# Kernel optimization log

Measured on AMD Instinct MI355X. Metric: run time of the kernel, lower is better.

## Reference

```python
import jax, jax.numpy as jnp
import numpy as np

N = 20000          # total nodes across batched graphs
E_REL = 60000      # edges per relation type (3 relation types)
N_CLASSES = 32
NUM_GRAPHS = 64
HEADS = 8
OUT_CH = 48
FUSED = 384        # 3 * 128 fused node feature dim
EPS = 1e-5         # PyG LayerNorm eps
NEG_SLOPE = 0.2    # RGATConv leaky_relu slope
NUM_ITERS = 2


def setup_inputs() -> dict:
    key = jax.random.key(0)
    ks = iter(jax.random.split(key, 48))

    def nrm(shape, scale=0.05):
        return jax.random.normal(next(ks), shape, jnp.float32) * scale

    inp = {}
    inp["x_visual"] = jax.random.normal(next(ks), (N, 1024), jnp.float32)
    inp["x_geom"] = jax.random.normal(next(ks), (N, 6), jnp.float32)
    inp["x_prior"] = jax.random.uniform(next(ks), (N, N_CLASSES + 1), jnp.float32)
    inp["edge_index_overlap"] = jax.random.randint(next(ks), (2, E_REL), 0, N)
    inp["edge_index_arch"] = jax.random.randint(next(ks), (2, E_REL), 0, N)
    inp["edge_index_spatial"] = jax.random.randint(next(ks), (2, E_REL), 0, N)
    inp["batch"] = jnp.sort(jax.random.randint(next(ks), (N,), 0, NUM_GRAPHS))
    # encoders: Linear -> ReLU -> PyG LayerNorm(graph mode, batch=None)
    inp["vis_W"] = nrm((1024, 128)); inp["vis_b"] = jnp.zeros((128,), jnp.float32)
    inp["vis_lnw"] = jnp.ones((128,), jnp.float32); inp["vis_lnb"] = jnp.zeros((128,), jnp.float32)
    inp["geo_W"] = nrm((6, 128)); inp["geo_b"] = jnp.zeros((128,), jnp.float32)
    inp["geo_lnw"] = jnp.ones((128,), jnp.float32); inp["geo_lnb"] = jnp.zeros((128,), jnp.float32)
    inp["pri_W"] = nrm((N_CLASSES + 1, 128)); inp["pri_b"] = jnp.zeros((128,), jnp.float32)
    inp["pri_lnw"] = jnp.ones((128,), jnp.float32); inp["pri_lnb"] = jnp.zeros((128,), jnp.float32)
    # RGATConv params: weight (R, in, H*O), q/k (H*O, H*dim) with dim=1, bias (H*O)
    for i in (1, 2):
        inp[f"rgat{i}_W"] = nrm((3, FUSED, HEADS * OUT_CH))
        inp[f"rgat{i}_q"] = nrm((HEADS * OUT_CH, HEADS))
        inp[f"rgat{i}_k"] = nrm((HEADS * OUT_CH, HEADS))
        inp[f"rgat{i}_bias"] = jnp.zeros((HEADS * OUT_CH,), jnp.float32)
        inp[f"n{i}_w"] = jnp.ones((FUSED,), jnp.float32)
        inp[f"n{i}_b"] = jnp.zeros((FUSED,), jnp.float32)
    inp["cls_W1"] = nrm((FUSED, 128)); inp["cls_b1"] = jnp.zeros((128,), jnp.float32)
    inp["cls_W2"] = nrm((128, N_CLASSES)); inp["cls_b2"] = jnp.zeros((N_CLASSES,), jnp.float32)
    return inp


def _encoder(x, W, b, lnw, lnb):
    # Linear -> ReLU -> PyG LayerNorm(mode='graph', batch=None): scalar mean/std
    h = jax.nn.relu(x @ W + b)
    h = h - h.mean()
    h = h / (h.std() + EPS)
    return h * lnw + lnb


def _graph_layernorm(x, batch, w, b):
    # PyG LayerNorm(mode='graph') with batch vector: normalize per graph over nodes*channels
    cnt = jax.ops.segment_sum(jnp.ones((x.shape[0],), x.dtype), batch, NUM_GRAPHS)
    norm = jnp.clip(cnt, 1.0, None) * x.shape[-1]
    mean = jax.ops.segment_sum(x, batch, NUM_GRAPHS).sum(-1) / norm
    xc = x - mean[batch][:, None]
    var = jax.ops.segment_sum(xc * xc, batch, NUM_GRAPHS).sum(-1) / norm
    out = xc / jnp.sqrt(var + EPS)[batch][:, None]
    return out * w + b


def _rgat(x, src, dst, etype, W, q, k, bias):
    # RGATConv: additive self-attention, across-relation softmax, concat heads, sum aggr
    n = x.shape[0]
    xr = jnp.einsum('nf,rfo->rno', x, W)          # per-relation node transform (R,N,H*O)
    outi = xr[etype, dst]                          # (E, H*O) transformed dst features
    outj = xr[etype, src]                          # (E, H*O) transformed src features
    alpha = jax.nn.leaky_relu(outi @ q + outj @ k, NEG_SLOPE)  # (E, H)
    amax = jax.ops.segment_max(alpha, dst, n)
    amax = jnp.where(jnp.isfinite(amax), amax, 0.0)
    ex = jnp.exp(alpha - amax[dst])
    den = jax.ops.segment_sum(ex, dst, n)
    a = ex / (den[dst] + 1e-16)                    # per-dst-node softmax over all relations
    msg = (a[:, :, None] * outj.reshape(-1, HEADS, OUT_CH)).reshape(-1, HEADS * OUT_CH)
    return jax.ops.segment_sum(msg, dst, n) + bias


def reference(x_visual, x_geom, x_prior, edge_index_overlap, edge_index_arch,
              edge_index_spatial, batch, vis_W, vis_b, vis_lnw, vis_lnb,
              geo_W, geo_b, geo_lnw, geo_lnb, pri_W, pri_b, pri_lnw, pri_lnb,
              rgat1_W, rgat1_q, rgat1_k, rgat1_bias, n1_w, n1_b,
              rgat2_W, rgat2_q, rgat2_k, rgat2_bias, n2_w, n2_b,
              cls_W1, cls_b1, cls_W2, cls_b2):
    ei = jnp.concatenate([edge_index_overlap, edge_index_arch, edge_index_spatial], axis=1)
    src, dst = ei[0], ei[1]
    etype = jnp.concatenate([jnp.full((E_REL,), r, jnp.int32) for r in range(3)])

    h_vis = _encoder(x_visual, vis_W, vis_b, vis_lnw, vis_lnb)
    h_geo = _encoder(x_geom, geo_W, geo_b, geo_lnw, geo_lnb)

    cur_prior = x_prior
    logits = None
    for t in range(NUM_ITERS):
        h_pri = _encoder(cur_prior, pri_W, pri_b, pri_lnw, pri_lnb)
        h0 = jnp.concatenate([h_vis, h_geo, h_pri], axis=-1)  # (N, 384)
        h1 = jax.nn.elu(_rgat(h0, src, dst, etype, rgat1_W, rgat1_q, rgat1_k, rgat1_bias)) + h0
        h1 = _graph_layernorm(h1, batch, n1_w, n1_b)
        h2 = jax.nn.elu(_rgat(h1, src, dst, etype, rgat2_W, rgat2_q, rgat2_k, rgat2_bias)) + h1
        h2 = _graph_layernorm(h2, batch, n2_w, n2_b)
        logits = jax.nn.relu(h2 @ cls_W1 + cls_b1) @ cls_W2 + cls_b2  # dropout off (eval)
        if t < NUM_ITERS - 1:
            probs = jax.nn.softmax(logits, axis=-1)
            cur_prior = jnp.concatenate([probs, probs.max(-1, keepdims=True)], axis=-1)
    return logits
```

## Files before the change

kernel.cpp:

```cpp
#include <hip/hip_runtime.h>
#include <hip/hip_bf16.h>

#define Nn 20000
#define EREL 60000
#define ETOT 180000
#define NG 64
#define FD 384
#define EPS 1e-5f

typedef unsigned short u16;
typedef unsigned int u32;
typedef __attribute__((ext_vector_type(8))) short s8v;
typedef __attribute__((ext_vector_type(4))) float f4v;

static inline int cdiv(int a, int b) { return (a + b - 1) / b; }

__device__ inline u16 f2b(float f) {
    __hip_bfloat16 h = __float2bfloat16(f);
    union { __hip_bfloat16 b; u16 u; } c; c.b = h; return c.u;
}
__device__ inline float b2f(u16 u) {
    union { __hip_bfloat16 b; u16 u; } c; c.u = u; return __bfloat162float(c.b);
}

template<bool WLO>
__global__ __launch_bounds__(256) void split_k(const float* __restrict__ x,
    u16* __restrict__ hi, u16* __restrict__ lo, int n4)
{
    int i = blockIdx.x * 256 + threadIdx.x;
    if (i >= n4) return;
    float4 v = ((const float4*)x)[i];
    ushort4 h;
    h.x = f2b(v.x); h.y = f2b(v.y); h.z = f2b(v.z); h.w = f2b(v.w);
    ((ushort4*)hi)[i] = h;
    if (WLO) {
        ushort4 l;
        l.x = f2b(v.x - b2f(h.x));
        l.y = f2b(v.y - b2f(h.y));
        l.z = f2b(v.z - b2f(h.z));
        l.w = f2b(v.w - b2f(h.w));
        ((ushort4*)lo)[i] = l;
    }
}

template<bool WLO>
__global__ void tsplit_k(const float* __restrict__ W, u16* __restrict__ hi,
                         u16* __restrict__ lo, int K, int N, int total)
{
    int idx = blockIdx.x * 256 + threadIdx.x;
    if (idx >= total) return;
    int kn = K * N;
    int b = idx / kn, rem = idx - b * kn;
    int k = rem / N, n = rem - k * N;
    float v = W[idx];
    u16 h = f2b(v);
    int o = b * kn + n * K + k;
    hi[o] = h;
    if (WLO) lo[o] = f2b(v - b2f(h));
}

__global__ __launch_bounds__(256) void w2_k(const float* __restrict__ W0,
    const float* __restrict__ q0, const float* __restrict__ k0,
    const float* __restrict__ W1, const float* __restrict__ q1, const float* __restrict__ k1,
    u16* __restrict__ hi, u16* __restrict__ lo)
{
    int idx = blockIdx.x * 256 + threadIdx.x;
    if (idx >= 2 * 3 * 384 * 16) return;
    int c = idx & 15;
    int rest = idx >> 4;
    int kin = rest % 384;
    int lr3 = rest / 384;
    int L = lr3 / 3, r = lr3 - L * 3;
    const float* W = (L ? W1 : W0) + ((size_t)r * 384 + kin) * 384;
    const float* qm = (c < 8) ? (L ? q1 : q0) : (L ? k1 : k0);
    int h = c & 7;
    float s = 0.f;
    for (int d = 0; d < 384; d++) s = fmaf(W[d], qm[d * 8 + h], s);
    u16 hh = f2b(s);
    size_t o = ((size_t)L * 48 + r * 16 + c) * 384 + kin;
    hi[o] = hh;
    lo[o] = f2b(s - b2f(hh));
}

#define USEI(i) ((i) < 2 || ((i) >= 4 && (i) < 6) || (TERMS >= 2 && ((i) == 2 || (i) == 3)) || (TERMS >= 3 && (i) >= 6))
template<bool BIAS, bool RELU, bool STATS, bool OB16, int TERMS, bool SWZ>
__global__ __launch_bounds__(256) void mgemm_k(
    const u16* __restrict__ Ahi, const u16* __restrict__ Alo,
    const u16* __restrict__ Bhi, const u16* __restrict__ Blo,
    const float* __restrict__ bias, void* __restrict__ Cv,
    int M, int K, int ldc, int bstride, float* __restrict__ stats)
{
    __shared__ u16 lds[4 * 128 * 32];
    __shared__ float red[256];
    const int t = threadIdx.x;
    int brow, bcol, z;
    if (SWZ) {
        int d = blockIdx.x;
        int xcd = d & 7, s = d >> 3;
        int row = xcd + 8 * (s / 9);
        int c = s % 9;
        brow = row * 128;
        if (brow >= M) return;
        bcol = (c % 3) * 128;
        z = c / 3;
    } else {
        brow = blockIdx.x * 128; bcol = blockIdx.y * 128; z = blockIdx.z;
    }
    Bhi += (size_t)z * bstride;
    Blo += (size_t)z * bstride;
    float* Cf = OB16 ? nullptr : (float*)Cv + (size_t)z * M * ldc;
    u16*   Ch = OB16 ? (u16*)Cv + (size_t)z * M * ldc : nullptr;

    const int r0 = t >> 2, sl = t & 3;
    const int rA0 = min(brow + r0, M - 1);
    const int rA1 = min(brow + r0 + 64, M - 1);
    const u16* gsrc[8];
    gsrc[0] = Ahi + (size_t)rA0 * K + sl * 8;
    gsrc[1] = Ahi + (size_t)rA1 * K + sl * 8;
    gsrc[2] = Alo + (size_t)rA0 * K + sl * 8;
    gsrc[3] = Alo + (size_t)rA1 * K + sl * 8;
    gsrc[4] = Bhi + (size_t)(bcol + r0) * K + sl * 8;
    gsrc[5] = Bhi + (size_t)(bcol + r0 + 64) * K + sl * 8;
    gsrc[6] = Blo + (size_t)(bcol + r0) * K + sl * 8;
    gsrc[7] = Blo + (size_t)(bcol + r0 + 64) * K + sl * 8;
    const int swz = (sl ^ (r0 & 3)) << 3;
    int ldst[8];
    #pragma unroll
    for (int i = 0; i < 8; i++) {
        int tile = i >> 1, row = r0 + 64 * (i & 1);
        ldst[i] = tile * 4096 + row * 32 + swz;
    }

    const int l = t & 63, w = t >> 6;
    const int wr = (w >> 1) * 64, wc = (w & 1) * 64;
    const int lr = l & 15, kq = l >> 4;

    f4v acc[4][4] = {};
    const int NK = K >> 5;

    s8v stg[8];
    #pragma unroll
    for (int i = 0; i < 8; i++) if (USEI(i)) stg[i] = *(const s8v*)gsrc[i];

    for (int kc = 0; kc < NK; kc++) {
        if (kc) __syncthreads();
        #pragma unroll
        for (int i = 0; i < 8; i++) if (USEI(i)) *(s8v*)(lds + ldst[i]) = stg[i];
        __syncthreads();
        if (kc + 1 < NK) {
            const int ko = (kc + 1) * 32;
            #pragma unroll
            for (int i = 0; i < 8; i++) if (USEI(i)) stg[i] = *(const s8v*)(gsrc[i] + ko);
        }
        #define LDR(T, row) (*(const s8v*)(lds + (T) * 4096 + (row) * 32 + ((kq ^ ((row) & 3)) << 3)))
        s8v bh[4], bl[4];
        #pragma unroll
        for (int tn = 0; tn < 4; tn++) {
            int rb = wc + tn * 16 + lr;
            bh[tn] = LDR(2, rb);
            if (TERMS >= 3) bl[tn] = LDR(3, rb);
        }
        #pragma unroll
        for (int tm = 0; tm < 4; tm++) {
            int ra = wr + tm * 16 + lr;
            s8v ah = LDR(0, ra);
            s8v al;
            if (TERMS >= 2) al = LDR(1, ra);
            #pragma unroll
            for (int tn = 0; tn < 4; tn++) {
                acc[tm][tn] = __builtin_amdgcn_mfma_f32_16x16x32_bf16(ah, bh[tn], acc[tm][tn], 0, 0, 0);
                if (TERMS >= 2)
                    acc[tm][tn] = __builtin_amdgcn_mfma_f32_16x16x32_bf16(al, bh[tn], acc[tm][tn], 0, 0, 0);
                if (TERMS >= 3)
                    acc[tm][tn] = __builtin_amdgcn_mfma_f32_16x16x32_bf16(ah, bl[tn], acc[tm][tn], 0, 0, 0);
            }
        }
        #undef LDR
    }

    float s1 = 0.f, s2 = 0.f;
    #pragma unroll
    for (int tm = 0; tm < 4; tm++) {
        #pragma unroll
        for (int rg = 0; rg < 4; rg++) {
            int row = brow + wr + tm * 16 + kq * 4 + rg;
            if (row < M) {
                #pragma unroll
                for (int tn = 0; tn < 4; tn++) {
                    int col = bcol + wc + tn * 16 + lr;
                    float v = acc[tm][tn][rg];
                    if (BIAS) v += bias[col];
                    if (RELU) v = fmaxf(v, 0.f);
                    if (OB16) Ch[(size_t)row * ldc + col] = f2b(v);
                    else      Cf[(size_t)row * ldc + col] = v;
                    if (STATS) { s1 += v; s2 += v * v; }
                }
            }
        }
    }
    if (STATS) {
        __syncthreads();
        red[t] = s1; __syncthreads();
        for (int o = 128; o; o >>= 1) { if (t < o) red[t] += red[t + o]; __syncthreads(); }
        if (t == 0) atomicAdd(&stats[0], red[0]);
        __syncthreads();
        red[t] = s2; __syncthreads();
        for (int o = 128; o; o >>= 1) { if (t < o) red[t] += red[t + o]; __syncthreads(); }
        if (t == 0) atomicAdd(&stats[1], red[0]);
    }
}
#undef USEI

__global__ __launch_bounds__(256) void projh_k(const u16* __restrict__ hs,
    const u16* __restrict__ w2hi, const u16* __restrict__ w2lo, float* __restrict__ qik)
{
    __shared__ u16 a_lds[128 * 32];
    __shared__ u16 b_lds[2][48 * 392];
    int t = threadIdx.x;
    int brow = blockIdx.x * 128;

    for (int i = t; i < 2304; i += 256) {
        int col = i / 48, c8 = (i - col * 48) * 8;
        *(s8v*)&b_lds[0][col * 392 + c8] = *(const s8v*)(w2hi + col * 384 + c8);
        *(s8v*)&b_lds[1][col * 392 + c8] = *(const s8v*)(w2lo + col * 384 + c8);
    }

    int ar = t >> 1, sl0 = (t & 1) * 2;
    int grow = min(brow + ar, Nn - 1);
    const u16* asrc = hs + (size_t)grow * FD;
    int adst0 = ar * 32 + ((sl0 ^ (ar & 3)) << 3);
    int adst1 = ar * 32 + (((sl0 + 1) ^ (ar & 3)) << 3);

    int l = t & 63, w = t >> 6;
    int lr = l & 15, kq = l >> 4;
    f4v acc[2][3] = {};

    s8v stg0 = *(const s8v*)(asrc + sl0 * 8);
    s8v stg1 = *(const s8v*)(asrc + sl0 * 8 + 8);
    for (int kc = 0; kc < 12; kc++) {
        if (kc) __syncthreads();
        *(s8v*)&a_lds[adst0] = stg0;
        *(s8v*)&a_lds[adst1] = stg1;
        __syncthreads();
        if (kc + 1 < 12) {
            int ko = (kc + 1) * 32 + sl0 * 8;
            stg0 = *(const s8v*)(asrc + ko);
            stg1 = *(const s8v*)(asrc + ko + 8);
        }
        s8v bh[3], bl[3];
        #pragma unroll
        for (int cf = 0; cf < 3; cf++) {
            bh[cf] = *(const s8v*)&b_lds[0][(cf * 16 + lr) * 392 + kc * 32 + kq * 8];
            bl[cf] = *(const s8v*)&b_lds[1][(cf * 16 + lr) * 392 + kc * 32 + kq * 8];
        }
        #pragma unroll
        for (int rf = 0; rf < 2; rf++) {
            int rr = w * 32 + rf * 16 + lr;
            s8v a = *(const s8v*)&a_lds[rr * 32 + ((kq ^ (rr & 3)) << 3)];
            #pragma unroll
            for (int cf = 0; cf < 3; cf++) {
                acc[rf][cf] = __builtin_amdgcn_mfma_f32_16x16x32_bf16(a, bh[cf], acc[rf][cf], 0, 0, 0);
                acc[rf][cf] = __builtin_amdgcn_mfma_f32_16x16x32_bf16(a, bl[cf], acc[rf][cf], 0, 0, 0);
            }
        }
    }
    #pragma unroll
    for (int rf = 0; rf < 2; rf++)
        #pragma unroll
        for (int cf = 0; cf < 3; cf++)
            #pragma unroll
            for (int rg = 0; rg < 4; rg++) {
                int row = brow + w * 32 + rf * 16 + kq * 4 + rg;
                if (row < Nn) qik[(size_t)row * 48 + cf * 16 + lr] = acc[rf][cf][rg];
            }
}

template<bool BIAS, bool RELU, bool STATS>
__global__ __launch_bounds__(256) void sgemm_k(
    const float* __restrict__ A, const float* __restrict__ B,
    const float* __restrict__ bias, float* __restrict__ C,
    int M, int K, int N, int ldc, float* __restrict__ stats)
{
    const int BK = 16;
    const int r = blockIdx.z;
    B += (size_t)r * K * N;
    C += (size_t)r * M * ldc;
    __shared__ float As[16][65];
    __shared__ float Bs[16][64];
    int tid = threadIdx.x;
    int tx = tid & 15, ty = tid >> 4;
    int brow = blockIdx.x * 64, bcol = blockIdx.y * 64;
    float acc[4][4] = {};
    for (int k0 = 0; k0 < K; k0 += BK) {
        #pragma unroll
        for (int i = 0; i < 4; i++) {
            int e = tid + 256 * i;
            int ar = e >> 4, ak = e & 15;
            int gr = brow + ar, gk = k0 + ak;
            As[ak][ar] = (gr < M && gk < K) ? A[(size_t)gr * K + gk] : 0.f;
            int bk = e >> 6, bn = e & 63;
            int gbk = k0 + bk, gbn = bcol + bn;
            Bs[bk][bn] = (gbk < K && gbn < N) ? B[(size_t)gbk * N + gbn] : 0.f;
        }
        __syncthreads();
        #pragma unroll
        for (int k = 0; k < BK; k++) {
            float ra[4], rb[4];
            #pragma unroll
            for (int i = 0; i < 4; i++) ra[i] = As[k][ty * 4 + i];
            #pragma unroll
            for (int j = 0; j < 4; j++) rb[j] = Bs[k][tx * 4 + j];
            #pragma unroll
            for (int i = 0; i < 4; i++)
                #pragma unroll
                for (int j = 0; j < 4; j++)
                    acc[i][j] = fmaf(ra[i], rb[j], acc[i][j]);
        }
        __syncthreads();
    }
    float s1 = 0.f, s2 = 0.f;
    #pragma unroll
    for (int i = 0; i < 4; i++) {
        int row = brow + ty * 4 + i;
        #pragma unroll
        for (int j = 0; j < 4; j++) {
            int col = bcol + tx * 4 + j;
            if (row < M && col < N) {
                float v = acc[i][j];
                if (BIAS) v += bias[col];
                if (RELU) v = v > 0.f ? v : 0.f;
                C[(size_t)row * ldc + col] = v;
                if (STATS) { s1 += v; s2 += v * v; }
            }
        }
    }
    if (STATS) {
        __shared__ float red[256];
        __syncthreads();
        red[tid] = s1; __syncthreads();
        for (int o = 128; o; o >>= 1) { if (tid < o) red[tid] += red[tid + o]; __syncthreads(); }
        if (tid == 0) atomicAdd(&stats[0], red[0]);
        __syncthreads();
        red[tid] = s2; __syncthreads();
        for (int o = 128; o; o >>= 1) { if (tid < o) red[tid] += red[tid + o]; __syncthreads(); }
        if (tid == 0) atomicAdd(&stats[1], red[0]);
    }
}

__global__ __launch_bounds__(256) void enc_norm_k(const float* __restrict__ H,
                           const float* __restrict__ w, const float* __restrict__ b,
                           const float* __restrict__ stats, float cntinv, u16* __restrict__ hi)
{
    int i = blockIdx.x * 256 + threadIdx.x;
    if (i >= Nn * 32) return;
    int n = i >> 5, c4 = i & 31;
    float m = stats[0] * cntinv;
    float var = stats[1] * cntinv - m * m;
    float s = 1.f / (sqrtf(fmaxf(var, 0.f)) + EPS);
    float4 wv = ((const float4*)w)[c4];
    float4 bv = ((const float4*)b)[c4];
    float4 v = ((const float4*)(H + (size_t)n * FD))[c4];
    ushort4 hh;
    hh.x = f2b((v.x - m) * s * wv.x + bv.x);
    hh.y = f2b((v.y - m) * s * wv.y + bv.y);
    hh.z = f2b((v.z - m) * s * wv.z + bv.z);
    hh.w = f2b((v.w - m) * s * wv.w + bv.w);
    ((ushort4*)(hi + (size_t)n * FD))[c4] = hh;
}

__global__ void edge_count_k(const int* __restrict__ e0, const int* __restrict__ e1,
                             const int* __restrict__ e2, int* __restrict__ cnt)
{
    int e = blockIdx.x * 256 + threadIdx.x;
    if (e >= ETOT) return;
    int r = e / EREL, i = e - r * EREL;
    const int* ei = (r == 0) ? e0 : (r == 1) ? e1 : e2;
    atomicAdd(&cnt[ei[EREL + i]], 1);
}

__global__ void edge_fill_k(const int* __restrict__ e0, const int* __restrict__ e1,
                            const int* __restrict__ e2, int* __restrict__ cursor,
                            int* __restrict__ eidx)
{
    int e = blockIdx.x * 256 + threadIdx.x;
    if (e >= ETOT) return;
    int r = e / EREL, i = e - r * EREL;
    const int* ei = (r == 0) ? e0 : (r == 1) ? e1 : e2;
    int src = ei[i], dst = ei[EREL + i];
    int pos = atomicAdd(&cursor[dst], 1);
    eidx[pos] = src | (r << 24);
}

__global__ __launch_bounds__(1024) void scan_k(const int* __restrict__ cnt,
                                               int* __restrict__ rowptr, int* __restrict__ cursor)
{
    __shared__ int wsum[16], wpre[16];
    __shared__ int carry, tot;
    int t = threadIdx.x, lane = t & 63, wid = t >> 6;
    if (t == 0) carry = 0;
    __syncthreads();
    for (int base = 0; base < Nn; base += 1024) {
        int i = base + t;
        int v = (i < Nn) ? cnt[i] : 0;
        int s = v;
        #pragma unroll
        for (int o = 1; o < 64; o <<= 1) {
            int x = __shfl_up(s, o);
            if (lane >= o) s += x;
        }
        if (lane == 63) wsum[wid] = s;
        __syncthreads();
        if (t < 16) {
            int wv = wsum[t];
            int ws = wv;
            #pragma unroll
            for (int o = 1; o < 16; o <<= 1) {
                int x = __shfl_up(ws, o);
                if (t >= o) ws += x;
            }
            wpre[t] = ws - wv;
            if (t == 15) tot = ws;
        }
        __syncthreads();
        if (i < Nn) {
            int ex = carry + wpre[wid] + s - v;
            rowptr[i] = ex; cursor[i] = ex;
        }
        __syncthreads();
        if (t == 0) carry += tot;
    }
    __syncthreads();
    if (t == 0) rowptr[Nn] = carry;
}

__global__ __launch_bounds__(256) void gcount_k(const int* __restrict__ batch, int* __restrict__ gcnt)
{
    __shared__ int bins[NG];
    int t = threadIdx.x;
    if (t < NG) bins[t] = 0;
    __syncthreads();
    int n = blockIdx.x * 256 + t;
    if (n < Nn) atomicAdd(&bins[batch[n]], 1);
    __syncthreads();
    if (t < NG && bins[t]) atomicAdd(&gcnt[t], bins[t]);
}

__global__ __launch_bounds__(256) void aggr_k(const u16* __restrict__ xr,
    const float* __restrict__ qik, const int* __restrict__ rowptr, const int* __restrict__ eidx,
    const float* __restrict__ bias, const u16* __restrict__ hinb,
    const int* __restrict__ batch, u16* __restrict__ outb,
    float* __restrict__ gsum, float* __restrict__ gsq)
{
    __shared__ float ls[NG], lq[NG];
    int t = threadIdx.x;
    if (t < NG) { ls[t] = 0.f; lq[t] = 0.f; }
    __syncthreads();
    int node = blockIdx.x * 4 + (t >> 6);
    int lane = t & 63;
    int e0 = rowptr[node], e1 = rowptr[node + 1];
    int hd = lane >> 3;
    float qv = (lane < 48) ? qik[(size_t)node * 48 + lane] : 0.f;
    float den = 0.f;
    float acc[6] = {};

    int e = e0;
    while (e + 4 <= e1) {
        int p0 = eidx[e], p1 = eidx[e + 1], p2 = eidx[e + 2], p3 = eidx[e + 3];
        int n0 = p0 & 0xFFFFFF, et0 = p0 >> 24;
        int n1 = p1 & 0xFFFFFF, et1 = p1 >> 24;
        int n2 = p2 & 0xFFFFFF, et2 = p2 >> 24;
        int n3 = p3 & 0xFFFFFF, et3 = p3 >> 24;
        float kv0 = (lane < 8) ? qik[(size_t)n0 * 48 + et0 * 16 + 8 + lane] : 0.f;
        float kv1 = (lane < 8) ? qik[(size_t)n1 * 48 + et1 * 16 + 8 + lane] : 0.f;
        float kv2 = (lane < 8) ? qik[(size_t)n2 * 48 + et2 * 16 + 8 + lane] : 0.f;
        float kv3 = (lane < 8) ? qik[(size_t)n3 * 48 + et3 * 16 + 8 + lane] : 0.f;
        const u32* r0 = (const u32*)(xr + ((size_t)et0 * Nn + n0) * FD);
        const u32* r1 = (const u32*)(xr + ((size_t)et1 * Nn + n1) * FD);
        const u32* r2 = (const u32*)(xr + ((size_t)et2 * Nn + n2) * FD);
        const u32* r3 = (const u32*)(xr + ((size_t)et3 * Nn + n3) * FD);
        u32 u0[3], u1[3], u2[3], u3[3];
        #pragma unroll
        for (int j = 0; j < 3; j++) u0[j] = r0[lane * 3 + j];
        #pragma unroll
        for (int j = 0; j < 3; j++) u1[j] = r1[lane * 3 + j];
        #pragma unroll
        for (int j = 0; j < 3; j++) u2[j] = r2[lane * 3 + j];
        #pragma unroll
        for (int j = 0; j < 3; j++) u3[j] = r3[lane * 3 + j];
        float qq0 = __shfl(qv, et0 * 16 + (lane & 7));
        float qq1 = __shfl(qv, et1 * 16 + (lane & 7));
        float qq2 = __shfl(qv, et2 * 16 + (lane & 7));
        float qq3 = __shfl(qv, et3 * 16 + (lane & 7));
        float ex0 = 0.f, ex1 = 0.f, ex2 = 0.f, ex3 = 0.f;
        if (lane < 8) {
            float a0 = qq0 + kv0; a0 = (a0 > 0.f) ? a0 : 0.2f * a0; ex0 = __expf(a0);
            float a1 = qq1 + kv1; a1 = (a1 > 0.f) ? a1 : 0.2f * a1; ex1 = __expf(a1);
            float a2 = qq2 + kv2; a2 = (a2 > 0.f) ? a2 : 0.2f * a2; ex2 = __expf(a2);
            float a3 = qq3 + kv3; a3 = (a3 > 0.f) ? a3 : 0.2f * a3; ex3 = __expf(a3);
        }
        den += ex0 + ex1 + ex2 + ex3;
        float w0 = __shfl(ex0, hd), w1 = __shfl(ex1, hd);
        float w2 = __shfl(ex2, hd), w3 = __shfl(ex3, hd);
        #pragma unroll
        for (int j = 0; j < 3; j++) {
            acc[2*j]   = fmaf(w0, __uint_as_float(u0[j] << 16), acc[2*j]);
            acc[2*j+1] = fmaf(w0, __uint_as_float(u0[j] & 0xffff0000u), acc[2*j+1]);
            acc[2*j]   = fmaf(w1, __uint_as_float(u1[j] << 16), acc[2*j]);
            acc[2*j+1] = fmaf(w1, __uint_as_float(u1[j] & 0xffff0000u), acc[2*j+1]);
            acc[2*j]   = fmaf(w2, __uint_as_float(u2[j] << 16), acc[2*j]);
            acc[2*j+1] = fmaf(w2, __uint_as_float(u2[j] & 0xffff0000u), acc[2*j+1]);
            acc[2*j]   = fmaf(w3, __uint_as_float(u3[j] << 16), acc[2*j]);
            acc[2*j+1] = fmaf(w3, __uint_as_float(u3[j] & 0xffff0000u), acc[2*j+1]);
        }
        e += 4;
    }
    for (; e < e1; e++) {
        int p = eidx[e];
        int sn = p & 0xFFFFFF, et = p >> 24;
        float kv = (lane < 8) ? qik[(size_t)sn * 48 + et * 16 + 8 + lane] : 0.f;
        const u32* rr = (const u32*)(xr + ((size_t)et * Nn + sn) * FD);
        u32 u[3];
        #pragma unroll
        for (int j = 0; j < 3; j++) u[j] = rr[lane * 3 + j];
        float qq = __shfl(qv, et * 16 + (lane & 7));
        float ex = 0.f;
        if (lane < 8) { float a = qq + kv; a = (a > 0.f) ? a : 0.2f * a; ex = __expf(a); }
        den += ex;
        float wv_ = __shfl(ex, hd);
        #pragma unroll
        for (int j = 0; j < 3; j++) {
            acc[2*j]   = fmaf(wv_, __uint_as_float(u[j] << 16), acc[2*j]);
            acc[2*j+1] = fmaf(wv_, __uint_as_float(u[j] & 0xffff0000u), acc[2*j+1]);
        }
    }

    float dh = __shfl(den, hd);
    float rcp = 1.f / (dh + 1e-16f);
    const u32* hp = (const u32*)(hinb + (size_t)node * FD);
    u32* op = (u32*)(outb + (size_t)node * FD);
    float s1 = 0.f, s2 = 0.f;
    #pragma unroll
    for (int j = 0; j < 3; j++) {
        int c = lane * 6 + 2 * j;
        float2 bv = *(const float2*)(bias + c);
        u32 hb = hp[lane * 3 + j];
        float vx = acc[2*j] * rcp + bv.x;
        float vy = acc[2*j+1] * rcp + bv.y;
        vx = (vx > 0.f) ? vx : expm1f(vx);
        vy = (vy > 0.f) ? vy : expm1f(vy);
        vx += b2f((u16)(hb & 0xffffu));
        vy += b2f((u16)(hb >> 16));
        op[lane * 3 + j] = (u32)f2b(vx) | ((u32)f2b(vy) << 16);
        s1 += vx + vy; s2 += vx * vx + vy * vy;
    }
    #pragma unroll
    for (int o = 32; o; o >>= 1) { s1 += __shfl_down(s1, o); s2 += __shfl_down(s2, o); }
    int g = batch[node];
    if (lane == 0) { atomicAdd(&ls[g], s1); atomicAdd(&lq[g], s2); }
    __syncthreads();
    if (t < NG && (ls[t] != 0.f || lq[t] != 0.f)) {
        atomicAdd(&gsum[t], ls[t]);
        atomicAdd(&gsq[t], lq[t]);
    }
}

template<bool WLO>
__global__ __launch_bounds__(256) void gnorm_split_k(const u16* __restrict__ yb,
    const int* __restrict__ batch, const float* __restrict__ gsum, const float* __restrict__ gsq,
    const int* __restrict__ gcnt, const float* __restrict__ w, const float* __restrict__ b,
    u16* __restrict__ hi, u16* __restrict__ lo)
{
    int i = blockIdx.x * 256 + threadIdx.x;
    if (i >= Nn * (FD / 4)) return;
    int n = i / 96;
    int c4 = i - n * 96;
    int g = batch[n];
    float norm = fmaxf((float)gcnt[g], 1.f) * (float)FD;
    float m = gsum[g] / norm;
    float var = gsq[g] / norm - m * m;
    float rstd = rsqrtf(var + EPS);
    float4 wv = ((const float4*)w)[c4];
    float4 bv = ((const float4*)b)[c4];
    uint2 yv = ((const uint2*)yb)[i];
    float v0 = (b2f((u16)(yv.x & 0xffffu)) - m) * rstd * wv.x + bv.x;
    float v1 = (b2f((u16)(yv.x >> 16))     - m) * rstd * wv.y + bv.y;
    float v2 = (b2f((u16)(yv.y & 0xffffu)) - m) * rstd * wv.z + bv.z;
    float v3 = (b2f((u16)(yv.y >> 16))     - m) * rstd * wv.w + bv.w;
    ushort4 hh;
    hh.x = f2b(v0); hh.y = f2b(v1); hh.z = f2b(v2); hh.w = f2b(v3);
    ((ushort4*)hi)[i] = hh;
    if (WLO) {
        ushort4 ll;
        ll.x = f2b(v0 - b2f(hh.x));
        ll.y = f2b(v1 - b2f(hh.y));
        ll.z = f2b(v2 - b2f(hh.z));
        ll.w = f2b(v3 - b2f(hh.w));
        ((ushort4*)lo)[i] = ll;
    }
}

__global__ void softmax_prior_k(const float* __restrict__ logits, float* __restrict__ prior)
{
    int n = blockIdx.x * 8 + (threadIdx.x >> 5);
    int l = threadIdx.x & 31;
    if (n >= Nn) return;
    float v = logits[n * 32 + l];
    float m = v;
    #pragma unroll
    for (int o = 16; o; o >>= 1) m = fmaxf(m, __shfl_xor(m, o, 32));
    float e = __expf(v - m);
    float s = e;
    #pragma unroll
    for (int o = 16; o; o >>= 1) s += __shfl_xor(s, o, 32);
    prior[(size_t)n * 33 + l] = e / s;
    if (l == 0) prior[(size_t)n * 33 + 32] = 1.f / s;
}

extern "C" void kernel_launch(void* const* d_in, const int* in_sizes, int n_in,
                              void* d_out, int out_size, void* d_ws, size_t ws_size,
                              hipStream_t stream)
{
    const float* x_visual = (const float*)d_in[0];
    const float* x_geom   = (const float*)d_in[1];
    const float* x_prior  = (const float*)d_in[2];
    const int* ei0   = (const int*)d_in[3];
    const int* ei1   = (const int*)d_in[4];
    const int* ei2   = (const int*)d_in[5];
    const int* batch = (const int*)d_in[6];
    const float* vis_W = (const float*)d_in[7];  const float* vis_b = (const float*)d_in[8];
    const float* vis_lnw = (const float*)d_in[9]; const float* vis_lnb = (const float*)d_in[10];
    const float* geo_W = (const float*)d_in[11]; const float* geo_b = (const float*)d_in[12];
    const float* geo_lnw = (const float*)d_in[13]; const float* geo_lnb = (const float*)d_in[14];
    const float* pri_W = (const float*)d_in[15]; const float* pri_b = (const float*)d_in[16];
    const float* pri_lnw = (const float*)d_in[17]; const float* pri_lnb = (const float*)d_in[18];
    const float* rgat_W[2]    = { (const float*)d_in[19], (const float*)d_in[25] };
    const float* rgat_q[2]    = { (const float*)d_in[20], (const float*)d_in[26] };
    const float* rgat_kk[2]   = { (const float*)d_in[21], (const float*)d_in[27] };
    const float* rgat_bias[2] = { (const float*)d_in[22], (const float*)d_in[28] };
    const float* ln_w[2]      = { (const float*)d_in[23], (const float*)d_in[29] };
    const float* ln_b[2]      = { (const float*)d_in[24], (const float*)d_in[30] };
    const float* cls_W1 = (const float*)d_in[31]; const float* cls_b1 = (const float*)d_in[32];
    const float* cls_W2 = (const float*)d_in[33]; const float* cls_b2 = (const float*)d_in[34];
    float* OUT = (float*)d_out;

    float* ws = (float*)d_ws;
    float* XRreg = ws;
    u16*   XR16  = (u16*)XRreg;
    float* HCAT  = XRreg + (size_t)3 * Nn * FD;
    float* HA    = HCAT + (size_t)Nn * FD;
    float* HB    = HA + (size_t)Nn * FD;
    float* PRIOR = HB + (size_t)Nn * FD;
    float* QIK   = PRIOR + (size_t)Nn * 33;
    u16* HS0_HI  = (u16*)(QIK + (size_t)Nn * 48);
    u16* HS0_LO  = HS0_HI + (size_t)Nn * FD;
    u16* HS1_HI  = HS0_LO + (size_t)Nn * FD;
    u16* HS1_LO  = HS1_HI + (size_t)Nn * FD;
    u16* RW_HI   = HS1_LO + (size_t)Nn * FD;
    u16* RW_LO   = RW_HI + (size_t)2 * 3 * 384 * 384;
    u16* VW_HI   = RW_LO + (size_t)2 * 3 * 384 * 384;
    u16* VW_LO   = VW_HI + (size_t)128 * 1024;
    u16* CW_HI   = VW_LO + (size_t)128 * 1024;
    u16* CW_LO   = CW_HI + (size_t)128 * 384;
    u16* W2_HI   = CW_LO + (size_t)128 * 384;
    u16* W2_LO   = W2_HI + (size_t)2 * 48 * 384;
    float* STATS = (float*)(W2_LO + (size_t)2 * 48 * 384);
    float* GSUM  = STATS + 2;
    float* GSQ   = GSUM + 64;
    int* CNT    = (int*)(GSQ + 64);
    int* ROWPTR = CNT + Nn;
    int* CURSOR = ROWPTR + Nn + 1;
    int* EIDX   = CURSOR + Nn;
    int* GCNT   = EIDX + ETOT;
    u16* VA_HI = (u16*)XRreg;
    float* CLSH = XRreg;
    u16* HS2_HI = (u16*)(XRreg + (size_t)12 * 1000 * 1000);
    u16* HS2_LO = HS2_HI + (size_t)Nn * FD;
    u16* YB0 = (u16*)HA;
    u16* YB1 = (u16*)HB;

    hipMemsetAsync(CNT, 0, Nn * sizeof(int), stream);
    edge_count_k<<<cdiv(ETOT, 256), 256, 0, stream>>>(ei0, ei1, ei2, CNT);
    scan_k<<<1, 1024, 0, stream>>>(CNT, ROWPTR, CURSOR);
    edge_fill_k<<<cdiv(ETOT, 256), 256, 0, stream>>>(ei0, ei1, ei2, CURSOR, EIDX);
    hipMemsetAsync(GCNT, 0, 64 * sizeof(int), stream);
    gcount_k<<<cdiv(Nn, 256), 256, 0, stream>>>(batch, GCNT);

    tsplit_k<false><<<cdiv(3 * 384 * 384, 256), 256, 0, stream>>>(rgat_W[0], RW_HI, RW_LO, 384, 384, 3 * 384 * 384);
    tsplit_k<false><<<cdiv(3 * 384 * 384, 256), 256, 0, stream>>>(rgat_W[1], RW_HI + 3 * 384 * 384, RW_LO, 384, 384, 3 * 384 * 384);
    tsplit_k<false><<<cdiv(1024 * 128, 256), 256, 0, stream>>>(vis_W, VW_HI, VW_LO, 1024, 128, 1024 * 128);
    tsplit_k<true><<<cdiv(384 * 128, 256), 256, 0, stream>>>(cls_W1, CW_HI, CW_LO, 384, 128, 384 * 128);
    w2_k<<<cdiv(2 * 3 * 384 * 16, 256), 256, 0, stream>>>(rgat_W[0], rgat_q[0], rgat_kk[0],
        rgat_W[1], rgat_q[1], rgat_kk[1], W2_HI, W2_LO);
    split_k<false><<<cdiv(Nn * 1024 / 4, 256), 256, 0, stream>>>(x_visual, VA_HI, nullptr, Nn * 1024 / 4);

    const int MB = cdiv(Nn, 128);
    const int XRBLK = 160 * 9;

    hipMemsetAsync(STATS, 0, 2 * sizeof(float), stream);
    mgemm_k<true, true, true, false, 1, false><<<dim3(MB, 1, 1), 256, 0, stream>>>(
        VA_HI, VA_HI, VW_HI, VW_LO, vis_b, HCAT, Nn, 1024, FD, 0, STATS);
    enc_norm_k<<<cdiv(Nn * 32, 256), 256, 0, stream>>>(HCAT, vis_lnw, vis_lnb, STATS, 1.f / ((float)Nn * 128.f), HS0_HI);

    dim3 genc(cdiv(Nn, 64), 2, 1);
    hipMemsetAsync(STATS, 0, 2 * sizeof(float), stream);
    sgemm_k<true, true, true><<<genc, 256, 0, stream>>>(x_geom, geo_W, geo_b, HCAT + 128, Nn, 6, 128, FD, STATS);
    enc_norm_k<<<cdiv(Nn * 32, 256), 256, 0, stream>>>(HCAT + 128, geo_lnw, geo_lnb, STATS, 1.f / ((float)Nn * 128.f), HS0_HI + 128);

    for (int t = 0; t < 2; t++) {
        const float* pin = t ? PRIOR : x_prior;
        hipMemsetAsync(STATS, 0, 2 * sizeof(float), stream);
        sgemm_k<true, true, true><<<genc, 256, 0, stream>>>(pin, pri_W, pri_b, HCAT + 256, Nn, 33, 128, FD, STATS);
        enc_norm_k<<<cdiv(Nn * 32, 256), 256, 0, stream>>>(HCAT + 256, pri_lnw, pri_lnb, STATS, 1.f / ((float)Nn * 128.f), HS0_HI + 256);

        for (int L = 0; L < 2; L++) {
            const u16* ahi = L ? HS1_HI : HS0_HI;
            u16* yout = L ? YB1 : YB0;
            mgemm_k<false, false, false, true, 1, true><<<dim3(XRBLK, 1, 1), 256, 0, stream>>>(
                ahi, ahi, RW_HI + (size_t)L * 3 * 384 * 384, RW_LO,
                nullptr, XR16, Nn, 384, FD, 384 * 384, nullptr);
            projh_k<<<MB, 256, 0, stream>>>(ahi,
                W2_HI + (size_t)L * 48 * 384, W2_LO + (size_t)L * 48 * 384, QIK);
            hipMemsetAsync(GSUM, 0, 128 * sizeof(float), stream);
            aggr_k<<<cdiv(Nn, 4), 256, 0, stream>>>(XR16, QIK, ROWPTR, EIDX, rgat_bias[L],
                                                    ahi, batch, yout, GSUM, GSQ);
            if (L == 0)
                gnorm_split_k<false><<<cdiv(Nn * 96, 256), 256, 0, stream>>>(
                    YB0, batch, GSUM, GSQ, GCNT, ln_w[0], ln_b[0], HS1_HI, HS1_LO);
            else
                gnorm_split_k<true><<<cdiv(Nn * 96, 256), 256, 0, stream>>>(
                    YB1, batch, GSUM, GSQ, GCNT, ln_w[1], ln_b[1], HS2_HI, HS2_LO);
        }

        mgemm_k<true, true, false, false, 3, false><<<dim3(MB, 1, 1), 256, 0, stream>>>(
            HS2_HI, HS2_LO, CW_HI, CW_LO, cls_b1, CLSH, Nn, 384, 128, 0, nullptr);
        sgemm_k<true, false, false><<<dim3(cdiv(Nn, 64), 1, 1), 256, 0, stream>>>(
            CLSH, cls_W2, cls_b2, OUT, Nn, 128, 32, 32, nullptr);

        if (t == 0)
            softmax_prior_k<<<cdiv(Nn, 8), 256, 0, stream>>>(OUT, PRIOR);
    }
}
```

Measured before the change: 770.2 us.

## Fuse fp32-to-bf16 conversion into visual GEMM, add small encoder kernel, drop memsets

After: 738.1 us. -4.2%, faster.

```diff
diff --git a/kernel.cpp b/kernel.cpp
--- a/kernel.cpp
+++ b/kernel.cpp
@@ -21,26 +21,6 @@
 }
 __device__ inline float b2f(u16 u) {
     union { __hip_bfloat16 b; u16 u; } c; c.u = u; return __bfloat162float(c.b);
-}
-
-template<bool WLO>
-__global__ __launch_bounds__(256) void split_k(const float* __restrict__ x,
-    u16* __restrict__ hi, u16* __restrict__ lo, int n4)
-{
-    int i = blockIdx.x * 256 + threadIdx.x;
-    if (i >= n4) return;
-    float4 v = ((const float4*)x)[i];
-    ushort4 h;
-    h.x = f2b(v.x); h.y = f2b(v.y); h.z = f2b(v.z); h.w = f2b(v.w);
-    ((ushort4*)hi)[i] = h;
-    if (WLO) {
-        ushort4 l;
-        l.x = f2b(v.x - b2f(h.x));
-        l.y = f2b(v.y - b2f(h.y));
-        l.z = f2b(v.z - b2f(h.z));
-        l.w = f2b(v.w - b2f(h.w));
-        ((ushort4*)lo)[i] = l;
-    }
 }
 
 template<bool WLO>
@@ -64,28 +44,81 @@
     const float* __restrict__ W1, const float* __restrict__ q1, const float* __restrict__ k1,
     u16* __restrict__ hi, u16* __restrict__ lo)
 {
-    int idx = blockIdx.x * 256 + threadIdx.x;
-    if (idx >= 2 * 3 * 384 * 16) return;
-    int c = idx & 15;
-    int rest = idx >> 4;
-    int kin = rest % 384;
-    int lr3 = rest / 384;
+    int row = blockIdx.x * 4 + (threadIdx.x >> 6);
+    int lane = threadIdx.x & 63;
+    if (row >= 2304) return;
+    int kin = row % 384;
+    int lr3 = row / 384;
     int L = lr3 / 3, r = lr3 - L * 3;
     const float* W = (L ? W1 : W0) + ((size_t)r * 384 + kin) * 384;
-    const float* qm = (c < 8) ? (L ? q1 : q0) : (L ? k1 : k0);
-    int h = c & 7;
-    float s = 0.f;
-    for (int d = 0; d < 384; d++) s = fmaf(W[d], qm[d * 8 + h], s);
-    u16 hh = f2b(s);
-    size_t o = ((size_t)L * 48 + r * 16 + c) * 384 + kin;
-    hi[o] = hh;
-    lo[o] = f2b(s - b2f(hh));
+    const float* qm = L ? q1 : q0;
+    const float* km = L ? k1 : k0;
+    float pq[16] = {};
+    #pragma unroll
+    for (int j = 0; j < 6; j++) {
+        int d = lane + 64 * j;
+        float x = W[d];
+        #pragma unroll
+        for (int h = 0; h < 8; h++) {
+            pq[h]     = fmaf(x, qm[d * 8 + h], pq[h]);
+            pq[8 + h] = fmaf(x, km[d * 8 + h], pq[8 + h]);
+        }
+    }
+    #pragma unroll
+    for (int o = 32; o; o >>= 1) {
+        #pragma unroll
+        for (int h = 0; h < 16; h++) pq[h] += __shfl_down(pq[h], o);
+    }
+    if (lane == 0) {
+        #pragma unroll
+        for (int c = 0; c < 16; c++) {
+            u16 hh = f2b(pq[c]);
+            size_t o = ((size_t)L * 48 + r * 16 + c) * 384 + kin;
+            hi[o] = hh; lo[o] = f2b(pq[c] - b2f(hh));
+        }
+    }
+}
+
+__global__ __launch_bounds__(256) void enc_gemm_k(const float* __restrict__ x, int K,
+    const float* __restrict__ W, const float* __restrict__ bias,
+    u16* __restrict__ out, float* __restrict__ stats)
+{
+    __shared__ float Wl[33 * 128];
+    __shared__ float bl[128];
+    __shared__ float red[8];
+    int t = threadIdx.x;
+    for (int i = t; i < K * 128; i += 256) Wl[i] = W[i];
+    if (t < 128) bl[t] = bias[t];
+    __syncthreads();
+    int wid = t >> 6, lane = t & 63;
+    float s1 = 0.f, s2 = 0.f;
+    for (int rr = 0; rr < 8; rr++) {
+        int n = blockIdx.x * 32 + wid * 8 + rr;
+        if (n >= Nn) break;
+        float xv = (lane < K) ? x[(size_t)n * K + lane] : 0.f;
+        float a0 = 0.f, a1 = 0.f;
+        for (int k = 0; k < K; k++) {
+            float xk = __shfl(xv, k);
+            a0 = fmaf(xk, Wl[k * 128 + 2 * lane], a0);
+            a1 = fmaf(xk, Wl[k * 128 + 2 * lane + 1], a1);
+        }
+        a0 = fmaxf(a0 + bl[2 * lane], 0.f);
+        a1 = fmaxf(a1 + bl[2 * lane + 1], 0.f);
+        ((u32*)(out + (size_t)n * FD))[lane] = (u32)f2b(a0) | ((u32)f2b(a1) << 16);
+        s1 += a0 + a1; s2 += a0 * a0 + a1 * a1;
+    }
+    #pragma unroll
+    for (int o = 32; o; o >>= 1) { s1 += __shfl_down(s1, o); s2 += __shfl_down(s2, o); }
+    if (lane == 0) { red[wid] = s1; red[4 + wid] = s2; }
+    __syncthreads();
+    if (t == 0) atomicAdd(&stats[0], red[0] + red[1] + red[2] + red[3]);
+    if (t == 1) atomicAdd(&stats[1], red[4] + red[5] + red[6] + red[7]);
 }
 
 #define USEI(i) ((i) < 2 || ((i) >= 4 && (i) < 6) || (TERMS >= 2 && ((i) == 2 || (i) == 3)) || (TERMS >= 3 && (i) >= 6))
-template<bool BIAS, bool RELU, bool STATS, bool OB16, int TERMS, bool SWZ>
+template<bool BIAS, bool RELU, bool STATS, bool OB16, int TERMS, bool SWZ, bool AF32>
 __global__ __launch_bounds__(256) void mgemm_k(
-    const u16* __restrict__ Ahi, const u16* __restrict__ Alo,
+    const u16* __restrict__ Ahi, const u16* __restrict__ Alo, const float* __restrict__ Af,
     const u16* __restrict__ Bhi, const u16* __restrict__ Blo,
     const float* __restrict__ bias, void* __restrict__ Cv,
     int M, int K, int ldc, int bstride, float* __restrict__ stats)
@@ -123,6 +156,11 @@
     gsrc[5] = Bhi + (size_t)(bcol + r0 + 64) * K + sl * 8;
     gsrc[6] = Blo + (size_t)(bcol + r0) * K + sl * 8;
     gsrc[7] = Blo + (size_t)(bcol + r0 + 64) * K + sl * 8;
+    const float* afsrc[2];
+    if (AF32) {
+        afsrc[0] = Af + (size_t)rA0 * K + sl * 8;
+        afsrc[1] = Af + (size_t)rA1 * K + sl * 8;
+    }
     const int swz = (sl ^ (r0 & 3)) << 3;
     int ldst[8];
     #pragma unroll
@@ -138,9 +176,22 @@
     f4v acc[4][4] = {};
     const int NK = K >> 5;
 
+    #define LDA32(i, ko) ({ \
+        float4 f0_ = *(const float4*)(afsrc[i] + (ko)); \
+        float4 f1_ = *(const float4*)(afsrc[i] + (ko) + 4); \
+        s8v r_; \
+        r_[0] = (short)f2b(f0_.x); r_[1] = (short)f2b(f0_.y); \
+        r_[2] = (short)f2b(f0_.z); r_[3] = (short)f2b(f0_.w); \
+        r_[4] = (short)f2b(f1_.x); r_[5] = (short)f2b(f1_.y); \
+        r_[6] = (short)f2b(f1_.z); r_[7] = (short)f2b(f1_.w); \
+        r_; })
+
     s8v stg[8];
     #pragma unroll
-    for (int i = 0; i < 8; i++) if (USEI(i)) stg[i] = *(const s8v*)gsrc[i];
+    for (int i = 0; i < 8; i++) {
+        if (AF32 && i < 2) stg[i] = LDA32(i, 0);
+        else if (!(AF32 && i < 2) && USEI(i)) stg[i] = *(const s8v*)gsrc[i];
+    }
 
     for (int kc = 0; kc < NK; kc++) {
         if (kc) __syncthreads();
@@ -150,7 +201,10 @@
         if (kc + 1 < NK) {
             const int ko = (kc + 1) * 32;
             #pragma unroll
-            for (int i = 0; i < 8; i++) if (USEI(i)) stg[i] = *(const s8v*)(gsrc[i] + ko);
+            for (int i = 0; i < 8; i++) {
+                if (AF32 && i < 2) stg[i] = LDA32(i, ko);
+                else if (!(AF32 && i < 2) && USEI(i)) stg[i] = *(const s8v*)(gsrc[i] + ko);
+            }
         }
         #define LDR(T, row) (*(const s8v*)(lds + (T) * 4096 + (row) * 32 + ((kq ^ ((row) & 3)) << 3)))
         s8v bh[4], bl[4];
@@ -177,6 +231,7 @@
         }
         #undef LDR
     }
+    #undef LDA32
 
     float s1 = 0.f, s2 = 0.f;
     #pragma unroll
@@ -275,16 +330,13 @@
             }
 }
 
-template<bool BIAS, bool RELU, bool STATS>
+template<bool BIAS, bool RELU>
 __global__ __launch_bounds__(256) void sgemm_k(
     const float* __restrict__ A, const float* __restrict__ B,
     const float* __restrict__ bias, float* __restrict__ C,
-    int M, int K, int N, int ldc, float* __restrict__ stats)
+    int M, int K, int N, int ldc)
 {
     const int BK = 16;
-    const int r = blockIdx.z;
-    B += (size_t)r * K * N;
-    C += (size_t)r * M * ldc;
     __shared__ float As[16][65];
     __shared__ float Bs[16][64];
     int tid = threadIdx.x;
@@ -318,7 +370,6 @@
         }
         __syncthreads();
     }
-    float s1 = 0.f, s2 = 0.f;
     #pragma unroll
     for (int i = 0; i < 4; i++) {
         int row = brow + ty * 4 + i;
@@ -330,24 +381,12 @@
                 if (BIAS) v += bias[col];
                 if (RELU) v = v > 0.f ? v : 0.f;
                 C[(size_t)row * ldc + col] = v;
-                if (STATS) { s1 += v; s2 += v * v; }
             }
         }
     }
-    if (STATS) {
-        __shared__ float red[256];
-        __syncthreads();
-        red[tid] = s1; __syncthreads();
-        for (int o = 128; o; o >>= 1) { if (tid < o) red[tid] += red[tid + o]; __syncthreads(); }
-        if (tid == 0) atomicAdd(&stats[0], red[0]);
-        __syncthreads();
-        red[tid] = s2; __syncthreads();
-        for (int o = 128; o; o >>= 1) { if (tid < o) red[tid] += red[tid + o]; __syncthreads(); }
-        if (tid == 0) atomicAdd(&stats[1], red[0]);
-    }
-}
-
-__global__ __launch_bounds__(256) void enc_norm_k(const float* __restrict__ H,
+}
+
+__global__ __launch_bounds__(256) void enc_norm_k(const u16* __restrict__ H,
                            const float* __restrict__ w, const float* __restrict__ b,
                            const float* __restrict__ stats, float cntinv, u16* __restrict__ hi)
 {
@@ -359,12 +398,12 @@
     float s = 1.f / (sqrtf(fmaxf(var, 0.f)) + EPS);
     float4 wv = ((const float4*)w)[c4];
     float4 bv = ((const float4*)b)[c4];
-    float4 v = ((const float4*)(H + (size_t)n * FD))[c4];
+    uint2 yv = ((const uint2*)(H + (size_t)n * FD))[c4];
     ushort4 hh;
-    hh.x = f2b((v.x - m) * s * wv.x + bv.x);
-    hh.y = f2b((v.y - m) * s * wv.y + bv.y);
-    hh.z = f2b((v.z - m) * s * wv.z + bv.z);
-    hh.w = f2b((v.w - m) * s * wv.w + bv.w);
+    hh.x = f2b((b2f((u16)(yv.x & 0xffffu)) - m) * s * wv.x + bv.x);
+    hh.y = f2b((b2f((u16)(yv.x >> 16))     - m) * s * wv.y + bv.y);
+    hh.z = f2b((b2f((u16)(yv.y & 0xffffu)) - m) * s * wv.z + bv.z);
+    hh.w = f2b((b2f((u16)(yv.y >> 16))     - m) * s * wv.w + bv.w);
     ((ushort4*)(hi + (size_t)n * FD))[c4] = hh;
 }
 
@@ -647,6 +686,7 @@
     float* XRreg = ws;
     u16*   XR16  = (u16*)XRreg;
     float* HCAT  = XRreg + (size_t)3 * Nn * FD;
+    u16*   HENC  = (u16*)HCAT;
     float* HA    = HCAT + (size_t)Nn * FD;
     float* HB    = HA + (size_t)Nn * FD;
     float* PRIOR = HB + (size_t)Nn * FD;
@@ -663,15 +703,13 @@
     u16* CW_LO   = CW_HI + (size_t)128 * 384;
     u16* W2_HI   = CW_LO + (size_t)128 * 384;
     u16* W2_LO   = W2_HI + (size_t)2 * 48 * 384;
-    float* STATS = (float*)(W2_LO + (size_t)2 * 48 * 384);
-    float* GSUM  = STATS + 2;
-    float* GSQ   = GSUM + 64;
-    int* CNT    = (int*)(GSQ + 64);
+    float* GS    = (float*)(W2_LO + (size_t)2 * 48 * 384);
+    float* STATS = GS + 512;
+    int* CNT    = (int*)(STATS + 8);
     int* ROWPTR = CNT + Nn;
     int* CURSOR = ROWPTR + Nn + 1;
     int* EIDX   = CURSOR + Nn;
     int* GCNT   = EIDX + ETOT;
-    u16* VA_HI = (u16*)XRreg;
     float* CLSH = XRreg;
     u16* HS2_HI = (u16*)(XRreg + (size_t)12 * 1000 * 1000);
     u16* HS2_LO = HS2_HI + (size_t)Nn * FD;
@@ -684,57 +722,54 @@
     edge_fill_k<<<cdiv(ETOT, 256), 256, 0, stream>>>(ei0, ei1, ei2, CURSOR, EIDX);
     hipMemsetAsync(GCNT, 0, 64 * sizeof(int), stream);
     gcount_k<<<cdiv(Nn, 256), 256, 0, stream>>>(batch, GCNT);
+    hipMemsetAsync(GS, 0, 520 * sizeof(float), stream);
 
     tsplit_k<false><<<cdiv(3 * 384 * 384, 256), 256, 0, stream>>>(rgat_W[0], RW_HI, RW_LO, 384, 384, 3 * 384 * 384);
     tsplit_k<false><<<cdiv(3 * 384 * 384, 256), 256, 0, stream>>>(rgat_W[1], RW_HI + 3 * 384 * 384, RW_LO, 384, 384, 3 * 384 * 384);
     tsplit_k<false><<<cdiv(1024 * 128, 256), 256, 0, stream>>>(vis_W, VW_HI, VW_LO, 1024, 128, 1024 * 128);
     tsplit_k<true><<<cdiv(384 * 128, 256), 256, 0, stream>>>(cls_W1, CW_HI, CW_LO, 384, 128, 384 * 128);
-    w2_k<<<cdiv(2 * 3 * 384 * 16, 256), 256, 0, stream>>>(rgat_W[0], rgat_q[0], rgat_kk[0],
-        rgat_W[1], rgat_q[1], rgat_kk[1], W2_HI, W2_LO);
-    split_k<false><<<cdiv(Nn * 1024 / 4, 256), 256, 0, stream>>>(x_visual, VA_HI, nullptr, Nn * 1024 / 4);
+    w2_k<<<576, 256, 0, stream>>>(rgat_W[0], rgat_q[0], rgat_kk[0],
+                                  rgat_W[1], rgat_q[1], rgat_kk[1], W2_HI, W2_LO);
 
     const int MB = cdiv(Nn, 128);
     const int XRBLK = 160 * 9;
-
-    hipMemsetAsync(STATS, 0, 2 * sizeof(float), stream);
-    mgemm_k<true, true, true, false, 1, false><<<dim3(MB, 1, 1), 256, 0, stream>>>(
-        VA_HI, VA_HI, VW_HI, VW_LO, vis_b, HCAT, Nn, 1024, FD, 0, STATS);
-    enc_norm_k<<<cdiv(Nn * 32, 256), 256, 0, stream>>>(HCAT, vis_lnw, vis_lnb, STATS, 1.f / ((float)Nn * 128.f), HS0_HI);
-
-    dim3 genc(cdiv(Nn, 64), 2, 1);
-    hipMemsetAsync(STATS, 0, 2 * sizeof(float), stream);
-    sgemm_k<true, true, true><<<genc, 256, 0, stream>>>(x_geom, geo_W, geo_b, HCAT + 128, Nn, 6, 128, FD, STATS);
-    enc_norm_k<<<cdiv(Nn * 32, 256), 256, 0, stream>>>(HCAT + 128, geo_lnw, geo_lnb, STATS, 1.f / ((float)Nn * 128.f), HS0_HI + 128);
+    const float cinv = 1.f / ((float)Nn * 128.f);
+
+    mgemm_k<true, true, true, true, 1, false, true><<<dim3(MB, 1, 1), 256, 0, stream>>>(
+        nullptr, nullptr, x_visual, VW_HI, VW_LO, vis_b, HENC, Nn, 1024, FD, 0, STATS + 0);
+    enc_norm_k<<<cdiv(Nn * 32, 256), 256, 0, stream>>>(HENC, vis_lnw, vis_lnb, STATS + 0, cinv, HS0_HI);
+
+    enc_gemm_k<<<cdiv(Nn, 32), 256, 0, stream>>>(x_geom, 6, geo_W, geo_b, HENC + 128, STATS + 2);
+    enc_norm_k<<<cdiv(Nn * 32, 256), 256, 0, stream>>>(HENC + 128, geo_lnw, geo_lnb, STATS + 2, cinv, HS0_HI + 128);
 
     for (int t = 0; t < 2; t++) {
         const float* pin = t ? PRIOR : x_prior;
-        hipMemsetAsync(STATS, 0, 2 * sizeof(float), stream);
-        sgemm_k<true, true, true><<<genc, 256, 0, stream>>>(pin, pri_W, pri_b, HCAT + 256, Nn, 33, 128, FD, STATS);
-        enc_norm_k<<<cdiv(Nn * 32, 256), 256, 0, stream>>>(HCAT + 256, pri_lnw, pri_lnb, STATS, 1.f / ((float)Nn * 128.f), HS0_HI + 256);
+        enc_gemm_k<<<cdiv(Nn, 32), 256, 0, stream>>>(pin, 33, pri_W, pri_b, HENC + 256, STATS + 4 + 2 * t);
+        enc_norm_k<<<cdiv(Nn * 32, 256), 256, 0, stream>>>(HENC + 256, pri_lnw, pri_lnb, STATS + 4 + 2 * t, cinv, HS0_HI + 256);
 
         for (int L = 0; L < 2; L++) {
             const u16* ahi = L ? HS1_HI : HS0_HI;
             u16* yout = L ? YB1 : YB0;
-            mgemm_k<false, false, false, true, 1, true><<<dim3(XRBLK, 1, 1), 256, 0, stream>>>(
-                ahi, ahi, RW_HI + (size_t)L * 3 * 384 * 384, RW_LO,
+            float* gsum = GS + (t * 2 + L) * 128;
+            mgemm_k<false, false, false, true, 1, true, false><<<dim3(XRBLK, 1, 1), 256, 0, stream>>>(
+                ahi, ahi, nullptr, RW_HI + (size_t)L * 3 * 384 * 384, RW_LO,
                 nullptr, XR16, Nn, 384, FD, 384 * 384, nullptr);
             projh_k<<<MB, 256, 0, stream>>>(ahi,
                 W2_HI + (size_t)L * 48 * 384, W2_LO + (size_t)L * 48 * 384, QIK);
-            hipMemsetAsync(GSUM, 0, 128 * sizeof(float), stream);
             aggr_k<<<cdiv(Nn, 4), 256, 0, stream>>>(XR16, QIK, ROWPTR, EIDX, rgat_bias[L],
-                                                    ahi, batch, yout, GSUM, GSQ);
+                                                    ahi, batch, yout, gsum, gsum + 64);
             if (L == 0)
                 gnorm_split_k<false><<<cdiv(Nn * 96, 256), 256, 0, stream>>>(
-                    YB0, batch, GSUM, GSQ, GCNT, ln_w[0], ln_b[0], HS1_HI, HS1_LO);
+                    YB0, batch, gsum, gsum + 64, GCNT, ln_w[0], ln_b[0], HS1_HI, HS1_LO);
             else
                 gnorm_split_k<true><<<cdiv(Nn * 96, 256), 256, 0, stream>>>(
-                    YB1, batch, GSUM, GSQ, GCNT, ln_w[1], ln_b[1], HS2_HI, HS2_LO);
-        }
-
-        mgemm_k<true, true, false, false, 3, false><<<dim3(MB, 1, 1), 256, 0, stream>>>(
-            HS2_HI, HS2_LO, CW_HI, CW_LO, cls_b1, CLSH, Nn, 384, 128, 0, nullptr);
-        sgemm_k<true, false, false><<<dim3(cdiv(Nn, 64), 1, 1), 256, 0, stream>>>(
-            CLSH, cls_W2, cls_b2, OUT, Nn, 128, 32, 32, nullptr);
+                    YB1, batch, gsum, gsum + 64, GCNT, ln_w[1], ln_b[1], HS2_HI, HS2_LO);
+        }
+
+        mgemm_k<true, true, false, false, 3, false, false><<<dim3(MB, 1, 1), 256, 0, stream>>>(
+            HS2_HI, HS2_LO, nullptr, CW_HI, CW_LO, cls_b1, CLSH, Nn, 384, 128, 0, nullptr);
+        sgemm_k<true, false><<<dim3(cdiv(Nn, 64), 1, 1), 256, 0, stream>>>(
+            CLSH, cls_W2, cls_b2, OUT, Nn, 128, 32, 32);
 
         if (t == 0)
             softmax_prior_k<<<cdiv(Nn, 8), 256, 0, stream>>>(OUT, PRIOR);
```
